# Optimization experiments

Hardware: AMD Instinct MI355X
Metric: run time of the kernel (lower is better)

## Reference

```python
import jax, jax.numpy as jnp
import numpy as np

B, N, C = 2, 8192, 768
H, K = 12, 256
D = C // H
HID = 4 * C
EPS = 1e-6

def layer_norm(x, w, b):
    mu = jnp.mean(x, axis=-1, keepdims=True)
    var = jnp.mean(jnp.square(x - mu), axis=-1, keepdims=True)
    return (x - mu) * jax.lax.rsqrt(var + EPS) * w + b

def setup_inputs() -> dict:
    key = jax.random.key(0)
    ks = jax.random.split(key, 8)
    s = 0.02
    return {
        "x": jax.random.normal(ks[0], (B, N, C), jnp.float32),
        "ln1_w": jnp.ones((C,), jnp.float32),
        "ln1_b": jnp.zeros((C,), jnp.float32),
        "qkv_w": jax.random.normal(ks[1], (C, 3 * C), jnp.float32) * s,
        "qkv_b": jnp.zeros((3 * C,), jnp.float32),
        "Ek": jax.random.normal(ks[2], (N, K), jnp.float32) * s,
        "Ev": jax.random.normal(ks[3], (N, K), jnp.float32) * s,
        "proj_w": jax.random.normal(ks[4], (C, C), jnp.float32) * s,
        "proj_b": jnp.zeros((C,), jnp.float32),
        "ln2_w": jnp.ones((C,), jnp.float32),
        "ln2_b": jnp.zeros((C,), jnp.float32),
        "fc1_w": jax.random.normal(ks[5], (C, HID), jnp.float32) * s,
        "fc1_b": jnp.zeros((HID,), jnp.float32),
        "fc2_w": jax.random.normal(ks[6], (HID, C), jnp.float32) * s,
        "fc2_b": jnp.zeros((C,), jnp.float32),
    }

def reference(x, ln1_w, ln1_b, qkv_w, qkv_b, Ek, Ev, proj_w, proj_b,
              ln2_w, ln2_b, fc1_w, fc1_b, fc2_w, fc2_b):
    scale = D ** -0.5
    # --- attention branch ---
    h = layer_norm(x, ln1_w, ln1_b)
    qkv = h @ qkv_w + qkv_b                      # (B,N,3C)
    qkv = qkv.reshape(B, N, 3, H, D).transpose(2, 0, 3, 1, 4)  # (3,B,H,N,D)
    q, k, v = qkv[0], qkv[1], qkv[2]
    # Linformer: project K/V along sequence dim N -> K
    k_proj = jnp.einsum('bhnd,nk->bhkd', k, Ek)
    v_proj = jnp.einsum('bhnd,nk->bhkd', v, Ev)
    logits = jnp.einsum('bhnd,bhkd->bhnk', q, k_proj) * scale
    logits = jnp.clip(logits, -50.0, 50.0)
    attn = jax.nn.softmax(logits, axis=-1)
    o = jnp.einsum('bhnk,bhkd->bhnd', attn, v_proj)
    o = o.transpose(0, 2, 1, 3).reshape(B, N, C)
    o = o @ proj_w + proj_b
    x = x + o                                    # alpha_attn = 1.0
    # --- MLP branch ---
    h = layer_norm(x, ln2_w, ln2_b)
    h = jax.nn.gelu(h @ fc1_w + fc1_b, approximate=False)
    h = h @ fc2_w + fc2_b
    return x + h                                 # alpha_mlp = 1.0
```

## Files before the change

kernel.cpp:

```cpp
#include <hip/hip_runtime.h>
#include <cstdint>

#define DEV __device__ __forceinline__

typedef __bf16 bf16x8 __attribute__((ext_vector_type(8)));
typedef float f32x4 __attribute__((ext_vector_type(4)));

DEV uint16_t f2bf(float f) {
  uint32_t u = __float_as_uint(f);
  u += 0x7FFFu + ((u >> 16) & 1u);
  return (uint16_t)(u >> 16);
}
DEV float bf2f(uint16_t h) { return __uint_as_float(((uint32_t)h) << 16); }

DEV void gload16(const void* g, void* l) {
  __builtin_amdgcn_global_load_lds((const __attribute__((address_space(1))) void*)g,
                                   (__attribute__((address_space(3))) void*)l, 16, 0, 0);
}

template <int N> DEV void waitcnt_vm() {
  if constexpr (N == 0) asm volatile("s_waitcnt vmcnt(0)" ::: "memory");
  else if constexpr (N == 3) asm volatile("s_waitcnt vmcnt(3)" ::: "memory");
  else if constexpr (N == 4) asm volatile("s_waitcnt vmcnt(4)" ::: "memory");
  else if constexpr (N == 8) asm volatile("s_waitcnt vmcnt(8)" ::: "memory");
  else static_assert(N == 0 || N == 3 || N == 4 || N == 8, "unsupported vmcnt");
}

DEV float gelu_f(float v) {
  float u = v * (0.7978845608f + 0.0356774081f * v * v);
  return v / (1.f + __expf(-2.f * u));
}

__global__ __launch_bounds__(256) void ln768(const float* __restrict__ x,
                                             const float* __restrict__ w,
                                             const float* __restrict__ b,
                                             uint16_t* __restrict__ out) {
  const size_t row = blockIdx.x;
  const float* xr = x + row * 768;
  const int t = threadIdx.x;
  float v0 = xr[t], v1 = xr[t + 256], v2 = xr[t + 512];
  float s = v0 + v1 + v2;
  float s2 = v0 * v0 + v1 * v1 + v2 * v2;
#pragma unroll
  for (int o = 32; o; o >>= 1) {
    s += __shfl_down(s, o);
    s2 += __shfl_down(s2, o);
  }
  __shared__ float sh[8];
  if ((t & 63) == 0) { sh[t >> 6] = s; sh[4 + (t >> 6)] = s2; }
  __syncthreads();
  s = sh[0] + sh[1] + sh[2] + sh[3];
  s2 = sh[4] + sh[5] + sh[6] + sh[7];
  const float mu = s * (1.f / 768.f);
  const float var = s2 * (1.f / 768.f) - mu * mu;
  const float rstd = rsqrtf(var + 1e-6f);
  uint16_t* orow = out + row * 768;
  orow[t]       = f2bf((v0 - mu) * rstd * w[t] + b[t]);
  orow[t + 256] = f2bf((v1 - mu) * rstd * w[t + 256] + b[t + 256]);
  orow[t + 512] = f2bf((v2 - mu) * rstd * w[t + 512] + b[t + 512]);
}

__global__ __launch_bounds__(256) void transpose_f2b(const float* __restrict__ in,
                                                     uint16_t* __restrict__ outp,
                                                     int ldin, int ldout) {
  __shared__ float tile[32][33];
  const int tx = threadIdx.x, ty = threadIdx.y;
  const size_t x = (size_t)blockIdx.x * 32 + tx;
  const size_t y = (size_t)blockIdx.y * 32 + ty;
#pragma unroll
  for (int j = 0; j < 4; ++j) tile[ty + j * 8][tx] = in[(y + j * 8) * ldin + x];
  __syncthreads();
  const size_t x2 = (size_t)blockIdx.y * 32 + tx;
  const size_t y2 = (size_t)blockIdx.x * 32 + ty;
#pragma unroll
  for (int j = 0; j < 4; ++j) outp[(y2 + j * 8) * ldout + x2] = f2bf(tile[tx][ty + j * 8]);
}

__global__ __launch_bounds__(256) void colsumE(const float* __restrict__ Ek,
                                               const float* __restrict__ Ev,
                                               float* __restrict__ colsum) {
  const int b = blockIdx.x;
  const float* src = (b < 4) ? Ek : Ev;
  const int kbase = (b & 3) * 64;
  const int kk = threadIdx.x & 63, s = threadIdx.x >> 6;
  float sum = 0.f;
  for (int i = 0; i < 2048; ++i)
    sum += src[(size_t)(s * 2048 + i) * 256 + kbase + kk];
  __shared__ float red[4][64];
  red[s][kk] = sum;
  __syncthreads();
  if (s == 0)
    colsum[(b >> 2) * 256 + kbase + kk] = (red[0][kk] + red[1][kk]) + (red[2][kk] + red[3][kk]);
}

__global__ __launch_bounds__(256) void hkv_tn(const float* __restrict__ Ek,
                                              const float* __restrict__ Ev,
                                              const uint16_t* __restrict__ h,
                                              float* __restrict__ part) {
  const int bid = blockIdx.x;
  const int wg = (bid & 7) * 96 + (bid >> 3);
  const int inner = wg & 31;
  const int kt = inner & 7, ns = inner >> 3;
  const int rest = wg >> 5;
  const int ct = rest % 12, b = rest / 12;
  const int k0 = kt * 64, c0 = ct * 64, nsb = ns * 2048;

  const float* Esrc = (k0 < 256) ? Ek : Ev;
  const int kc = k0 & 255;

  const int tid = threadIdx.x, wave = tid >> 6, lane = tid & 63;
  const int l16 = lane & 15, lhi = lane >> 4;
  const int wm = wave >> 1, wn = wave & 1;

  f32x4 acc[2][2];
#pragma unroll
  for (int m = 0; m < 2; ++m)
#pragma unroll
    for (int n = 0; n < 2; ++n) acc[m][n] = f32x4{0.f, 0.f, 0.f, 0.f};

  const int krow0 = kc + wm * 32 + l16;
  const uint16_t* Hb = h + ((size_t)b * 8192 + nsb + lhi * 8) * 768 + c0 + wn * 32 + l16;

  for (int n0 = 0; n0 < 2048; n0 += 32) {
    bf16x8 ef[2];
#pragma unroll
    for (int m = 0; m < 2; ++m) {
      const float* p = Esrc + (size_t)(nsb + n0 + lhi * 8) * 256 + krow0 + m * 16;
      union { bf16x8 v; uint16_t u[8]; } tu;
#pragma unroll
      for (int j = 0; j < 8; ++j) tu.u[j] = f2bf(p[(size_t)j * 256]);
      ef[m] = tu.v;
    }
    bf16x8 vf[2];
#pragma unroll
    for (int nf = 0; nf < 2; ++nf) {
      const uint16_t* p = Hb + (size_t)n0 * 768 + nf * 16;
      union { bf16x8 v; uint16_t u[8]; } tu;
#pragma unroll
      for (int j = 0; j < 8; ++j) tu.u[j] = p[(size_t)j * 768];
      vf[nf] = tu.v;
    }
#pragma unroll
    for (int m = 0; m < 2; ++m)
#pragma unroll
      for (int nf = 0; nf < 2; ++nf)
        acc[m][nf] = __builtin_amdgcn_mfma_f32_16x16x32_bf16(ef[m], vf[nf], acc[m][nf], 0, 0, 0);
  }

  float* outp = part + ((size_t)ns * 2 + b) * 393216;
#pragma unroll
  for (int m = 0; m < 2; ++m)
#pragma unroll
    for (int nf = 0; nf < 2; ++nf)
#pragma unroll
      for (int r = 0; r < 4; ++r)
        outp[(size_t)(k0 + wm * 32 + m * 16 + lhi * 4 + r) * 768 + c0 + wn * 32 + nf * 16 + l16] =
            acc[m][nf][r];
}

__global__ __launch_bounds__(256) void kv_reduce(const float* __restrict__ part,
                                                 uint16_t* __restrict__ hkv) {
  const int i = blockIdx.x * 256 + threadIdx.x;
  float s = part[i] + part[786432 + i] + part[2 * 786432 + i] + part[3 * 786432 + i];
  hkv[i] = f2bf(s);
}

template <int BM, int BN>
__global__ __launch_bounds__(256) void gemm_kvw(
    const uint16_t* __restrict__ Abase, const uint16_t* __restrict__ Bbase,
    uint16_t* __restrict__ Cbase, const float* __restrict__ bias,
    const float* __restrict__ rowscale, uint16_t* __restrict__ vpt,
    int Kd, int lda, int ldb, int ldc,
    int zdiv, size_t sAhi, size_t sAlo, size_t sBhi, size_t sBlo,
    size_t sChi, size_t sClo, int rs_z, int bias_z) {
  const int z = blockIdx.z;
  const int zhi = z / zdiv, zlo = z - zhi * zdiv;
  const uint16_t* A = Abase + zhi * sAhi + zlo * sAlo;
  const uint16_t* B = Bbase + zhi * sBhi + zlo * sBlo;
  const size_t coff = zhi * sChi + zlo * sClo;

  constexpr int WTM = BM / 2, WTN = BN / 2;
  constexpr int FM = WTM / 16, FN = WTN / 16;
  const int tid = threadIdx.x;
  const int wave = tid >> 6, lane = tid & 63;
  const int wm = wave >> 1, wn = wave & 1;
  const int l16 = lane & 15, lhi = lane >> 4;

  __shared__ __align__(16) uint16_t sA[BM * 32];
  __shared__ __align__(16) uint16_t sB[BN * 32];

  f32x4 acc[FM][FN];
#pragma unroll
  for (int m = 0; m < FM; ++m)
#pragma unroll
    for (int n = 0; n < FN; ++n) acc[m][n] = f32x4{0.f, 0.f, 0.f, 0.f};

  const int row0 = blockIdx.x * BM;
  const int col0 = blockIdx.y * BN;
  const int rr = tid >> 2, cq = tid & 3;

  for (int k0 = 0; k0 < Kd; k0 += 32) {
    __syncthreads();
#pragma unroll
    for (int is = 0; is < BM / 64; ++is) {
      const uint16_t* g = A + (size_t)(row0 + is * 64 + rr) * lda + k0 + cq * 8;
      gload16(g, &sA[is * 2048 + tid * 8]);
    }
#pragma unroll
    for (int is = 0; is < BN / 64; ++is) {
      const uint16_t* g = B + (size_t)(col0 + is * 64 + rr) * ldb + k0 + cq * 8;
      gload16(g, &sB[is * 2048 + tid * 8]);
    }
    __syncthreads();

    bf16x8 af[FM], bq[FN];
#pragma unroll
    for (int m = 0; m < FM; ++m)
      af[m] = *(const bf16x8*)(&sA[(wm * WTM + m * 16 + l16) * 32 + lhi * 8]);
#pragma unroll
    for (int n = 0; n < FN; ++n)
      bq[n] = *(const bf16x8*)(&sB[(wn * WTN + n * 16 + l16) * 32 + lhi * 8]);
#pragma unroll
    for (int m = 0; m < FM; ++m)
#pragma unroll
      for (int n = 0; n < FN; ++n)
        acc[m][n] = __builtin_amdgcn_mfma_f32_16x16x32_bf16(af[m], bq[n], acc[m][n], 0, 0, 0);
  }

#pragma unroll
  for (int m = 0; m < FM; ++m) {
#pragma unroll
    for (int n = 0; n < FN; ++n) {
      const int col = col0 + wn * WTN + n * 16 + l16;
      const float bv = bias[zlo * bias_z + col];
#pragma unroll
      for (int r = 0; r < 4; ++r) {
        const int row = row0 + wm * WTM + m * 16 + lhi * 4 + r;
        float v = acc[m][n][r] + rowscale[zlo * rs_z + row] * bv;
        if (zlo == 1) {
          vpt[(size_t)zhi * 196608 + (size_t)col * 256 + row] = f2bf(v);
        } else {
          Cbase[coff + (size_t)row * ldc + col] = f2bf(v);
        }
      }
    }
  }
}

__global__ __launch_bounds__(256, 3) void attn_fused(
    const uint16_t* __restrict__ q, const uint16_t* __restrict__ kproj,
    const uint16_t* __restrict__ vprojT, uint16_t* __restrict__ o) {
  const int bh = blockIdx.y;
  const int b = bh / 12, h = bh % 12;
  const int n0 = blockIdx.x * 64;
  const int tid = threadIdx.x, wave = tid >> 6, lane = tid & 63;
  const int l16 = lane & 15, lhi = lane >> 4;
  const int wm = wave >> 1, wn = wave & 1;

  __shared__ __align__(16) uint16_t sP[64 * 256];
  __shared__ float redm[2][64], reds[2][64], recs[64];

  const uint16_t* Kp = kproj + (size_t)b * 196608 + h * 64;
  const uint16_t* Qp = q + ((size_t)b * 8192 + n0) * 768 + h * 64;
  const uint16_t* Vp = vprojT + ((size_t)b * 768 + h * 64) * 256;

  f32x4 st[8][2];
#pragma unroll
  for (int m = 0; m < 8; ++m)
#pragma unroll
    for (int nf = 0; nf < 2; ++nf) st[m][nf] = f32x4{0.f, 0.f, 0.f, 0.f};
#pragma unroll
  for (int ks = 0; ks < 2; ++ks) {
    bf16x8 kf[8], qf[2];
#pragma unroll
    for (int m = 0; m < 8; ++m) {
      const int kvi = wm * 128 + m * 16 + l16;
      kf[m] = *(const bf16x8*)(Kp + (size_t)kvi * 768 + ks * 32 + lhi * 8);
    }
#pragma unroll
    for (int nf = 0; nf < 2; ++nf) {
      const int n = wn * 32 + nf * 16 + l16;
      qf[nf] = *(const bf16x8*)(Qp + (size_t)n * 768 + ks * 32 + lhi * 8);
    }
#pragma unroll
    for (int m = 0; m < 8; ++m)
#pragma unroll
      for (int nf = 0; nf < 2; ++nf)
        st[m][nf] = __builtin_amdgcn_mfma_f32_16x16x32_bf16(kf[m], qf[nf], st[m][nf], 0, 0, 0);
  }

  float pmax[2] = {-50.f, -50.f};
#pragma unroll
  for (int m = 0; m < 8; ++m)
#pragma unroll
    for (int nf = 0; nf < 2; ++nf)
#pragma unroll
      for (int r = 0; r < 4; ++r) {
        float v = fminf(fmaxf(st[m][nf][r] * 0.125f, -50.f), 50.f);
        st[m][nf][r] = v;
        pmax[nf] = fmaxf(pmax[nf], v);
      }
#pragma unroll
  for (int nf = 0; nf < 2; ++nf) {
    pmax[nf] = fmaxf(pmax[nf], __shfl_xor(pmax[nf], 16));
    pmax[nf] = fmaxf(pmax[nf], __shfl_xor(pmax[nf], 32));
  }
  if (lhi == 0) {
#pragma unroll
    for (int nf = 0; nf < 2; ++nf) redm[wm][wn * 32 + nf * 16 + l16] = pmax[nf];
  }
  __syncthreads();
  float M[2];
#pragma unroll
  for (int nf = 0; nf < 2; ++nf) {
    const int col = wn * 32 + nf * 16 + l16;
    M[nf] = fmaxf(redm[0][col], redm[1][col]);
  }

  float psum[2] = {0.f, 0.f};
#pragma unroll
  for (int m = 0; m < 8; ++m) {
#pragma unroll
    for (int nf = 0; nf < 2; ++nf) {
      float e0 = __expf(st[m][nf][0] - M[nf]);
      float e1 = __expf(st[m][nf][1] - M[nf]);
      float e2 = __expf(st[m][nf][2] - M[nf]);
      float e3 = __expf(st[m][nf][3] - M[nf]);
      psum[nf] += (e0 + e1) + (e2 + e3);
      uint2 pk;
      pk.x = (uint32_t)f2bf(e0) | ((uint32_t)f2bf(e1) << 16);
      pk.y = (uint32_t)f2bf(e2) | ((uint32_t)f2bf(e3) << 16);
      const int n = wn * 32 + nf * 16 + l16;
      const int kvb2 = (wm * 128 + m * 16 + lhi * 4) * 2;
      *(uint2*)((char*)sP + n * 512 + (kvb2 ^ ((n & 7) << 4))) = pk;
    }
  }
#pragma unroll
  for (int nf = 0; nf < 2; ++nf) {
    psum[nf] += __shfl_xor(psum[nf], 16);
    psum[nf] += __shfl_xor(psum[nf], 32);
  }
  if (lhi == 0) {
#pragma unroll
    for (int nf = 0; nf < 2; ++nf) reds[wm][wn * 32 + nf * 16 + l16] = psum[nf];
  }
  __syncthreads();
  if (wm == 0 && lhi == 0) {
#pragma unroll
    for (int nf = 0; nf < 2; ++nf) {
      const int col = wn * 32 + nf * 16 + l16;
      recs[col] = 1.f / (reds[0][col] + reds[1][col]);
    }
  }
  __syncthreads();

  f32x4 pacc[2][2];
#pragma unroll
  for (int mf = 0; mf < 2; ++mf)
#pragma unroll
    for (int nf = 0; nf < 2; ++nf) pacc[mf][nf] = f32x4{0.f, 0.f, 0.f, 0.f};
#pragma unroll
  for (int ks = 0; ks < 8; ++ks) {
    bf16x8 pa[2], vb[2];
#pragma unroll
    for (int mf = 0; mf < 2; ++mf) {
      const int n = wm * 32 + mf * 16 + l16;
      pa[mf] = *(const bf16x8*)((char*)sP + n * 512 + ((ks * 64 + lhi * 16) ^ ((n & 7) << 4)));
    }
#pragma unroll
    for (int nf = 0; nf < 2; ++nf) {
      const int d = wn * 32 + nf * 16 + l16;
      vb[nf] = *(const bf16x8*)(Vp + (size_t)d * 256 + ks * 32 + lhi * 8);
    }
#pragma unroll
    for (int mf = 0; mf < 2; ++mf)
#pragma unroll
      for (int nf = 0; nf < 2; ++nf)
        pacc[mf][nf] = __builtin_amdgcn_mfma_f32_16x16x32_bf16(pa[mf], vb[nf], pacc[mf][nf], 0, 0, 0);
  }
  uint16_t* orow = o + ((size_t)b * 8192 + n0) * 768 + h * 64;
#pragma unroll
  for (int mf = 0; mf < 2; ++mf) {
#pragma unroll
    for (int r = 0; r < 4; ++r) {
      const int n = wm * 32 + mf * 16 + lhi * 4 + r;
      const float inv = recs[n];
#pragma unroll
      for (int nf = 0; nf < 2; ++nf) {
        const int d = wn * 32 + nf * 16 + l16;
        orow[(size_t)n * 768 + d] = f2bf(pacc[mf][nf][r] * inv);
      }
    }
  }
}

template <bool OUTBF, bool HASBIAS, bool DOGELU, bool HASRES>
__global__ __launch_bounds__(256, 2) void gemm128(
    const uint16_t* __restrict__ A, const uint16_t* __restrict__ B,
    void* __restrict__ Cbase, const float* __restrict__ bias,
    const float* __restrict__ res, int Kd, int lda, int ldb, int ldc) {
  constexpr int PL = 4096;
  __shared__ __align__(16) uint16_t lds[4 * 2 * PL];

  const int nn = gridDim.y;
  const int nwg = gridDim.x * gridDim.y;
  const int bid = blockIdx.y * gridDim.x + blockIdx.x;
  const int q = nwg >> 3, r8 = nwg & 7, xcd = bid & 7, idx = bid >> 3;
  const int wg = (xcd < r8 ? xcd * (q + 1) : r8 * (q + 1) + (xcd - r8) * q) + idx;
  const int bm = wg / nn, bn = wg % nn;
  const int row0 = bm * 128, col0 = bn * 128;

  const int tid = threadIdx.x;
  const int wave = tid >> 6, lane = tid & 63;
  const int wm = wave >> 1, wn = wave & 1;
  const int l16 = lane & 15, lhi = lane >> 4;
  const int srow = tid >> 2, sq = tid & 3;

  auto stage = [&](int buf, int t) {
    const int k0 = t * 32;
    uint16_t* sa = lds + buf * 2 * PL;
#pragma unroll
    for (int j = 0; j < 2; ++j) {
      const int rw = j * 64 + srow;
      const int sl = sq ^ ((rw >> 1) & 3);
      gload16(A + (size_t)(row0 + rw) * lda + k0 + sl * 8, sa + rw * 32 + sq * 8);
    }
#pragma unroll
    for (int j = 0; j < 2; ++j) {
      const int rw = j * 64 + srow;
      const int sl = sq ^ ((rw >> 1) & 3);
      gload16(B + (size_t)(col0 + rw) * ldb + k0 + sl * 8, sa + PL + rw * 32 + sq * 8);
    }
  };

  f32x4 acc[4][4];
#pragma unroll
  for (int m = 0; m < 4; ++m)
#pragma unroll
    for (int n = 0; n < 4; ++n) acc[m][n] = f32x4{0.f, 0.f, 0.f, 0.f};

  const int NT = Kd >> 5;
  stage(0, 0);
  stage(1, 1);
  stage(2, 2);

  for (int t = 0; t < NT; ++t) {
    if (t < NT - 2) waitcnt_vm<8>();
    else if (t == NT - 2) waitcnt_vm<4>();
    else waitcnt_vm<0>();
    __builtin_amdgcn_s_barrier();
    asm volatile("" ::: "memory");
    if (t + 3 < NT) stage((t + 3) & 3, t + 3);

    const uint16_t* sa = lds + (t & 3) * 2 * PL;
    const uint16_t* sb = sa + PL;
    bf16x8 af[4], bfv[4];
#pragma unroll
    for (int n = 0; n < 4; ++n) {
      const int rw = wn * 64 + n * 16 + l16;
      bfv[n] = *(const bf16x8*)(sb + rw * 32 + (lhi ^ ((rw >> 1) & 3)) * 8);
    }
#pragma unroll
    for (int m = 0; m < 4; ++m) {
      const int rw = wm * 64 + m * 16 + l16;
      af[m] = *(const bf16x8*)(sa + rw * 32 + (lhi ^ ((rw >> 1) & 3)) * 8);
    }
    __builtin_amdgcn_s_setprio(1);
#pragma unroll
    for (int m = 0; m < 4; ++m)
#pragma unroll
      for (int n = 0; n < 4; ++n)
        acc[m][n] = __builtin_amdgcn_mfma_f32_16x16x32_bf16(af[m], bfv[n], acc[m][n], 0, 0, 0);
    __builtin_amdgcn_s_setprio(0);
  }

  float* Cf = (float*)Cbase;
  uint16_t* Cb = (uint16_t*)Cbase;
#pragma unroll
  for (int m = 0; m < 4; ++m) {
#pragma unroll
    for (int n = 0; n < 4; ++n) {
      const int col = col0 + wn * 64 + n * 16 + l16;
      float bv = 0.f;
      if (HASBIAS) bv = bias[col];
#pragma unroll
      for (int r = 0; r < 4; ++r) {
        const int row = row0 + wm * 64 + m * 16 + lhi * 4 + r;
        float v = acc[m][n][r] + bv;
        if (DOGELU) v = gelu_f(v);
        const size_t cidx = (size_t)row * ldc + col;
        if (HASRES) v += res[cidx];
        if (OUTBF) Cb[cidx] = f2bf(v);
        else Cf[cidx] = v;
      }
    }
  }
}

template <bool OUTBF, bool HASBIAS, bool DOGELU, bool HASRES>
__global__ __launch_bounds__(512, 4) void gemm512(
    const uint16_t* __restrict__ A, const uint16_t* __restrict__ B,
    void* __restrict__ Cbase, const float* __restrict__ bias,
    const float* __restrict__ res, int Kd, int lda, int ldb, int ldc) {
  constexpr int APL = 8192, BPL = 4096;
  __shared__ __align__(16) uint16_t lds[3 * (APL + BPL)];

  const int nn = gridDim.y;
  const int nwg = gridDim.x * gridDim.y;
  const int bid = blockIdx.y * gridDim.x + blockIdx.x;
  const int q = nwg >> 3, r8 = nwg & 7, xcd = bid & 7, idx = bid >> 3;
  const int wg = (xcd < r8 ? xcd * (q + 1) : r8 * (q + 1) + (xcd - r8) * q) + idx;
  const int bm = wg / nn, bn = wg % nn;
  const int row0 = bm * 256, col0 = bn * 128;

  const int tid = threadIdx.x;
  const int wave = tid >> 6, lane = tid & 63;
  const int wm = wave >> 1, wn = wave & 1;
  const int l16 = lane & 15, lhi = lane >> 4;
  const int srow = tid >> 2, sq = tid & 3;

  auto stage = [&](int buf, int t) {
    const int k0 = t * 32;
    uint16_t* sa = lds + buf * (APL + BPL);
#pragma unroll
    for (int j = 0; j < 2; ++j) {
      const int rw = j * 128 + srow;
      const int sl = sq ^ ((rw >> 1) & 3);
      gload16(A + (size_t)(row0 + rw) * lda + k0 + sl * 8, sa + rw * 32 + sq * 8);
    }
    {
      const int rw = srow;
      const int sl = sq ^ ((rw >> 1) & 3);
      gload16(B + (size_t)(col0 + rw) * ldb + k0 + sl * 8, sa + APL + rw * 32 + sq * 8);
    }
  };

  f32x4 acc[4][4];
#pragma unroll
  for (int m = 0; m < 4; ++m)
#pragma unroll
    for (int n = 0; n < 4; ++n) acc[m][n] = f32x4{0.f, 0.f, 0.f, 0.f};

  const int NT = Kd >> 5;
  stage(0, 0);
  stage(1, 1);

  for (int t = 0; t < NT; ++t) {
    if (t < NT - 1) waitcnt_vm<3>();
    else waitcnt_vm<0>();
    __builtin_amdgcn_s_barrier();
    asm volatile("" ::: "memory");
    if (t + 2 < NT) stage((t + 2) % 3, t + 2);

    const uint16_t* sa = lds + (t % 3) * (APL + BPL);
    const uint16_t* sb = sa + APL;
    bf16x8 af[4], bfv[4];
#pragma unroll
    for (int n = 0; n < 4; ++n) {
      const int rw = wn * 64 + n * 16 + l16;
      bfv[n] = *(const bf16x8*)(sb + rw * 32 + (lhi ^ ((rw >> 1) & 3)) * 8);
    }
#pragma unroll
    for (int m = 0; m < 4; ++m) {
      const int rw = wm * 64 + m * 16 + l16;
      af[m] = *(const bf16x8*)(sa + rw * 32 + (lhi ^ ((rw >> 1) & 3)) * 8);
    }
    __builtin_amdgcn_s_setprio(1);
#pragma unroll
    for (int m = 0; m < 4; ++m)
#pragma unroll
      for (int n = 0; n < 4; ++n)
        acc[m][n] = __builtin_amdgcn_mfma_f32_16x16x32_bf16(af[m], bfv[n], acc[m][n], 0, 0, 0);
    __builtin_amdgcn_s_setprio(0);
  }

  float* Cf = (float*)Cbase;
  uint16_t* Cb = (uint16_t*)Cbase;
#pragma unroll
  for (int m = 0; m < 4; ++m) {
#pragma unroll
    for (int n = 0; n < 4; ++n) {
      const int col = col0 + wn * 64 + n * 16 + l16;
      float bv = 0.f;
      if (HASBIAS) bv = bias[col];
#pragma unroll
      for (int r = 0; r < 4; ++r) {
        const int row = row0 + wm * 64 + m * 16 + lhi * 4 + r;
        float v = acc[m][n][r] + bv;
        if (DOGELU) v = gelu_f(v);
        const size_t cidx = (size_t)row * ldc + col;
        if (HASRES) v += res[cidx];
        if (OUTBF) Cb[cidx] = f2bf(v);
        else Cf[cidx] = v;
      }
    }
  }
}

extern "C" void kernel_launch(void* const* d_in, const int* in_sizes, int n_in,
                              void* d_out, int out_size, void* d_ws, size_t ws_size,
                              hipStream_t stream) {
  const float* x      = (const float*)d_in[0];
  const float* ln1_w  = (const float*)d_in[1];
  const float* ln1_b  = (const float*)d_in[2];
  const float* qkv_w  = (const float*)d_in[3];
  const float* qkv_b  = (const float*)d_in[4];
  const float* Ek     = (const float*)d_in[5];
  const float* Ev     = (const float*)d_in[6];
  const float* proj_w = (const float*)d_in[7];
  const float* proj_b = (const float*)d_in[8];
  const float* ln2_w  = (const float*)d_in[9];
  const float* ln2_b  = (const float*)d_in[10];
  const float* fc1_w  = (const float*)d_in[11];
  const float* fc1_b  = (const float*)d_in[12];
  const float* fc2_w  = (const float*)d_in[13];
  const float* fc2_b  = (const float*)d_in[14];
  float* out = (float*)d_out;

  char* w8 = (char*)d_ws;
  size_t off = 0;
  auto take = [&](size_t bytes) { char* p = w8 + off; off += bytes; return p; };
  uint16_t* qkv_wT  = (uint16_t*)take(2304ull * 768 * 2);
  uint16_t* proj_wT = (uint16_t*)take(768ull * 768 * 2);
  uint16_t* fc1_wT  = (uint16_t*)take(3072ull * 768 * 2);
  uint16_t* fc2_wT  = (uint16_t*)take(768ull * 3072 * 2);
  uint16_t* h_bf    = (uint16_t*)take(16384ull * 768 * 2);
  uint16_t* q_bf    = (uint16_t*)take(16384ull * 768 * 2);
  uint16_t* big     = (uint16_t*)take(100663296ull);
  uint16_t* hkv_bf  = (uint16_t*)take(2ull * 512 * 768 * 2);
  uint16_t* kproj   = (uint16_t*)take(2ull * 256 * 768 * 2);
  uint16_t* vprojT  = (uint16_t*)take(2ull * 768 * 256 * 2);
  uint16_t* o_bf    = (uint16_t*)take(16384ull * 768 * 2);
  float* colsum     = (float*)take(512 * 4);
  float* part = (float*)big;
  (void)ws_size; (void)in_sizes; (void)n_in; (void)out_size;

  const dim3 tb(32, 8);
  transpose_f2b<<<dim3(72, 24), tb, 0, stream>>>(qkv_w, qkv_wT, 2304, 768);
  transpose_f2b<<<dim3(24, 24), tb, 0, stream>>>(proj_w, proj_wT, 768, 768);
  transpose_f2b<<<dim3(96, 24), tb, 0, stream>>>(fc1_w, fc1_wT, 3072, 768);
  transpose_f2b<<<dim3(24, 96), tb, 0, stream>>>(fc2_w, fc2_wT, 768, 3072);
  colsumE<<<8, 256, 0, stream>>>(Ek, Ev, colsum);
  ln768<<<16384, 256, 0, stream>>>(x, ln1_w, ln1_b, h_bf);
  gemm128<true, true, false, false><<<dim3(128, 6), 256, 0, stream>>>(
      h_bf, qkv_wT, q_bf, qkv_b, nullptr, 768, 768, 768, 768);
  hkv_tn<<<768, 256, 0, stream>>>(Ek, Ev, h_bf, part);
  kv_reduce<<<3072, 256, 0, stream>>>(part, hkv_bf);
  gemm_kvw<64, 64><<<dim3(4, 12, 4), 256, 0, stream>>>(
      hkv_bf, qkv_wT + 768ull * 768, kproj, qkv_b + 768, colsum, vprojT,
      768, 768, 768, 768,
      2, 512ull * 768, 256ull * 768, 0, 768ull * 768, 196608, 0, 256, 768);
  attn_fused<<<dim3(128, 24), 256, 0, stream>>>(q_bf, kproj, vprojT, o_bf);
  gemm128<false, true, false, true><<<dim3(128, 6), 256, 0, stream>>>(
      o_bf, proj_wT, out, proj_b, x, 768, 768, 768, 768);
  ln768<<<16384, 256, 0, stream>>>(out, ln2_w, ln2_b, h_bf);
  gemm512<true, true, true, false><<<dim3(64, 24), 512, 0, stream>>>(
      h_bf, fc1_wT, big, fc1_b, nullptr, 768, 768, 768, 3072);
  gemm128<false, true, false, true><<<dim3(128, 6), 256, 0, stream>>>(
      big, fc2_wT, out, fc2_b, out, 3072, 3072, 3072, 768);
}
```

Measured before the change: 543.8 us.

## Store residual in bf16, merge weight transposes, shrink gemm128 pipeline to 3 stages

```diff
diff --git a/kernel.cpp b/kernel.cpp
--- a/kernel.cpp
+++ b/kernel.cpp
@@ -22,8 +22,7 @@
   if constexpr (N == 0) asm volatile("s_waitcnt vmcnt(0)" ::: "memory");
   else if constexpr (N == 3) asm volatile("s_waitcnt vmcnt(3)" ::: "memory");
   else if constexpr (N == 4) asm volatile("s_waitcnt vmcnt(4)" ::: "memory");
-  else if constexpr (N == 8) asm volatile("s_waitcnt vmcnt(8)" ::: "memory");
-  else static_assert(N == 0 || N == 3 || N == 4 || N == 8, "unsupported vmcnt");
+  else static_assert(N == 0 || N == 3 || N == 4, "unsupported vmcnt");
 }
 
 DEV float gelu_f(float v) {
@@ -60,18 +59,59 @@
   orow[t + 512] = f2bf((v2 - mu) * rstd * w[t + 512] + b[t + 512]);
 }
 
-__global__ __launch_bounds__(256) void transpose_f2b(const float* __restrict__ in,
-                                                     uint16_t* __restrict__ outp,
-                                                     int ldin, int ldout) {
+__global__ __launch_bounds__(256) void ln768b(const uint16_t* __restrict__ x,
+                                              const float* __restrict__ w,
+                                              const float* __restrict__ b,
+                                              uint16_t* __restrict__ out) {
+  const size_t row = blockIdx.x;
+  const uint16_t* xr = x + row * 768;
+  const int t = threadIdx.x;
+  float v0 = bf2f(xr[t]), v1 = bf2f(xr[t + 256]), v2 = bf2f(xr[t + 512]);
+  float s = v0 + v1 + v2;
+  float s2 = v0 * v0 + v1 * v1 + v2 * v2;
+#pragma unroll
+  for (int o = 32; o; o >>= 1) {
+    s += __shfl_down(s, o);
+    s2 += __shfl_down(s2, o);
+  }
+  __shared__ float sh[8];
+  if ((t & 63) == 0) { sh[t >> 6] = s; sh[4 + (t >> 6)] = s2; }
+  __syncthreads();
+  s = sh[0] + sh[1] + sh[2] + sh[3];
+  s2 = sh[4] + sh[5] + sh[6] + sh[7];
+  const float mu = s * (1.f / 768.f);
+  const float var = s2 * (1.f / 768.f) - mu * mu;
+  const float rstd = rsqrtf(var + 1e-6f);
+  uint16_t* orow = out + row * 768;
+  orow[t]       = f2bf((v0 - mu) * rstd * w[t] + b[t]);
+  orow[t + 256] = f2bf((v1 - mu) * rstd * w[t + 256] + b[t + 256]);
+  orow[t + 512] = f2bf((v2 - mu) * rstd * w[t + 512] + b[t + 512]);
+}
+
+__global__ __launch_bounds__(256) void transpose_all(
+    const float* __restrict__ w0, const float* __restrict__ w1,
+    const float* __restrict__ w2, const float* __restrict__ w3,
+    uint16_t* __restrict__ o0, uint16_t* __restrict__ o1,
+    uint16_t* __restrict__ o2, uint16_t* __restrict__ o3) {
+  int bid = blockIdx.x;
+  const float* in;
+  uint16_t* outp;
+  int gx, ldin, ldout;
+  if (bid < 1728) { in = w0; outp = o0; gx = 72; ldin = 2304; ldout = 768; }
+  else if (bid < 2304) { bid -= 1728; in = w1; outp = o1; gx = 24; ldin = 768; ldout = 768; }
+  else if (bid < 4608) { bid -= 2304; in = w2; outp = o2; gx = 96; ldin = 3072; ldout = 768; }
+  else { bid -= 4608; in = w3; outp = o3; gx = 24; ldin = 768; ldout = 3072; }
+  const int bx = bid % gx, by = bid / gx;
+
   __shared__ float tile[32][33];
   const int tx = threadIdx.x, ty = threadIdx.y;
-  const size_t x = (size_t)blockIdx.x * 32 + tx;
-  const size_t y = (size_t)blockIdx.y * 32 + ty;
+  const size_t x = (size_t)bx * 32 + tx;
+  const size_t y = (size_t)by * 32 + ty;
 #pragma unroll
   for (int j = 0; j < 4; ++j) tile[ty + j * 8][tx] = in[(y + j * 8) * ldin + x];
   __syncthreads();
-  const size_t x2 = (size_t)blockIdx.y * 32 + tx;
-  const size_t y2 = (size_t)blockIdx.x * 32 + ty;
+  const size_t x2 = (size_t)by * 32 + tx;
+  const size_t y2 = (size_t)bx * 32 + ty;
 #pragma unroll
   for (int j = 0; j < 4; ++j) outp[(y2 + j * 8) * ldout + x2] = f2bf(tile[tx][ty + j * 8]);
 }
@@ -394,13 +434,13 @@
   }
 }
 
-template <bool OUTBF, bool HASBIAS, bool DOGELU, bool HASRES>
-__global__ __launch_bounds__(256, 2) void gemm128(
+template <bool OUTBF, bool HASBIAS, bool DOGELU, bool HASRES, bool RESBF>
+__global__ __launch_bounds__(256, 3) void gemm128(
     const uint16_t* __restrict__ A, const uint16_t* __restrict__ B,
     void* __restrict__ Cbase, const float* __restrict__ bias,
-    const float* __restrict__ res, int Kd, int lda, int ldb, int ldc) {
+    const void* __restrict__ res, int Kd, int lda, int ldb, int ldc) {
   constexpr int PL = 4096;
-  __shared__ __align__(16) uint16_t lds[4 * 2 * PL];
+  __shared__ __align__(16) uint16_t lds[3 * 2 * PL];
 
   const int nn = gridDim.y;
   const int nwg = gridDim.x * gridDim.y;
@@ -442,17 +482,15 @@
   const int NT = Kd >> 5;
   stage(0, 0);
   stage(1, 1);
-  stage(2, 2);
 
   for (int t = 0; t < NT; ++t) {
-    if (t < NT - 2) waitcnt_vm<8>();
-    else if (t == NT - 2) waitcnt_vm<4>();
+    if (t < NT - 1) waitcnt_vm<4>();
     else waitcnt_vm<0>();
     __builtin_amdgcn_s_barrier();
     asm volatile("" ::: "memory");
-    if (t + 3 < NT) stage((t + 3) & 3, t + 3);
-
-    const uint16_t* sa = lds + (t & 3) * 2 * PL;
+    if (t + 2 < NT) stage((t + 2) % 3, t + 2);
+
+    const uint16_t* sa = lds + (t % 3) * 2 * PL;
     const uint16_t* sb = sa + PL;
     bf16x8 af[4], bfv[4];
 #pragma unroll
@@ -476,6 +514,8 @@
 
   float* Cf = (float*)Cbase;
   uint16_t* Cb = (uint16_t*)Cbase;
+  const float* resf = (const float*)res;
+  const uint16_t* resb = (const uint16_t*)res;
 #pragma unroll
   for (int m = 0; m < 4; ++m) {
 #pragma unroll
@@ -489,7 +529,7 @@
         float v = acc[m][n][r] + bv;
         if (DOGELU) v = gelu_f(v);
         const size_t cidx = (size_t)row * ldc + col;
-        if (HASRES) v += res[cidx];
+        if (HASRES) v += RESBF ? bf2f(resb[cidx]) : resf[cidx];
         if (OUTBF) Cb[cidx] = f2bf(v);
         else Cf[cidx] = v;
       }
@@ -631,18 +671,16 @@
   uint16_t* kproj   = (uint16_t*)take(2ull * 256 * 768 * 2);
   uint16_t* vprojT  = (uint16_t*)take(2ull * 768 * 256 * 2);
   uint16_t* o_bf    = (uint16_t*)take(16384ull * 768 * 2);
+  uint16_t* x2_bf   = (uint16_t*)take(16384ull * 768 * 2);
   float* colsum     = (float*)take(512 * 4);
   float* part = (float*)big;
   (void)ws_size; (void)in_sizes; (void)n_in; (void)out_size;
 
-  const dim3 tb(32, 8);
-  transpose_f2b<<<dim3(72, 24), tb, 0, stream>>>(qkv_w, qkv_wT, 2304, 768);
-  transpose_f2b<<<dim3(24, 24), tb, 0, stream>>>(proj_w, proj_wT, 768, 768);
-  transpose_f2b<<<dim3(96, 24), tb, 0, stream>>>(fc1_w, fc1_wT, 3072, 768);
-  transpose_f2b<<<dim3(24, 96), tb, 0, stream>>>(fc2_w, fc2_wT, 768, 3072);
+  transpose_all<<<6912, dim3(32, 8), 0, stream>>>(
+      qkv_w, proj_w, fc1_w, fc2_w, qkv_wT, proj_wT, fc1_wT, fc2_wT);
   colsumE<<<8, 256, 0, stream>>>(Ek, Ev, colsum);
   ln768<<<16384, 256, 0, stream>>>(x, ln1_w, ln1_b, h_bf);
-  gemm128<true, true, false, false><<<dim3(128, 6), 256, 0, stream>>>(
+  gemm128<true, true, false, false, false><<<dim3(128, 6), 256, 0, stream>>>(
       h_bf, qkv_wT, q_bf, qkv_b, nullptr, 768, 768, 768, 768);
   hkv_tn<<<768, 256, 0, stream>>>(Ek, Ev, h_bf, part);
   kv_reduce<<<3072, 256, 0, stream>>>(part, hkv_bf);
@@ -651,11 +689,11 @@
       768, 768, 768, 768,
       2, 512ull * 768, 256ull * 768, 0, 768ull * 768, 196608, 0, 256, 768);
   attn_fused<<<dim3(128, 24), 256, 0, stream>>>(q_bf, kproj, vprojT, o_bf);
-  gemm128<false, true, false, true><<<dim3(128, 6), 256, 0, stream>>>(
-      o_bf, proj_wT, out, proj_b, x, 768, 768, 768, 768);
-  ln768<<<16384, 256, 0, stream>>>(out, ln2_w, ln2_b, h_bf);
+  gemm128<true, true, false, true, false><<<dim3(128, 6), 256, 0, stream>>>(
+      o_bf, proj_wT, x2_bf, proj_b, x, 768, 768, 768, 768);
+  ln768b<<<16384, 256, 0, stream>>>(x2_bf, ln2_w, ln2_b, h_bf);
   gemm512<true, true, true, false><<<dim3(64, 24), 512, 0, stream>>>(
       h_bf, fc1_wT, big, fc1_b, nullptr, 768, 768, 768, 3072);
-  gemm128<false, true, false, true><<<dim3(128, 6), 256, 0, stream>>>(
-      big, fc2_wT, out, fc2_b, out, 3072, 3072, 3072, 768);
-}
+  gemm128<false, true, false, true, true><<<dim3(128, 6), 256, 0, stream>>>(
+      big, fc2_wT, out, fc2_b, x2_bf, 3072, 3072, 3072, 768);
+}
```

Measured after the change: 527.7 us. -3.0%, faster.
